# Optimization experiments

Measured on AMD Instinct MI355X. Metric: run time of the kernel, lower is better.

## Reference

```python
import jax, jax.numpy as jnp
import numpy as np


def sparsemax(z):
    """Euclidean projection onto the simplex (Martins & Astudillo 2016).
    z: (..., L) logits -> sparse probability vectors of same shape.
    """
    L = z.shape[-1]
    z_sorted = jnp.flip(jnp.sort(z, axis=-1), axis=-1)          # descending
    cum = jnp.cumsum(z_sorted, axis=-1)
    k = jnp.arange(1, L + 1, dtype=z.dtype)                     # 1..L
    support = 1.0 + k * z_sorted > cum                          # prefix-true mask
    k_max = jnp.sum(support, axis=-1, keepdims=True).astype(z.dtype)
    # sum of z_sorted over the support == cumsum at the last supported index
    cum_at_k = jnp.sum(jnp.where(support, z_sorted, 0.0), axis=-1, keepdims=True)
    tau = (cum_at_k - 1.0) / k_max
    return jnp.maximum(z - tau, 0.0)


def setup_inputs() -> dict:
    key = jax.random.key(0)
    k1, k2 = jax.random.split(key)
    B, K, L = 64, 16, 16384
    attention_logits = jax.random.normal(k1, (B, K, L), dtype=jnp.float32)
    rationale_mask = (jax.random.uniform(k2, (B, L)) < 0.1).astype(jnp.float32)
    return {"attention_logits": attention_logits, "rationale_mask": rationale_mask}


def reference(attention_logits, rationale_mask):
    # normalize the rationale mask into a probability target q
    q = rationale_mask / jnp.clip(
        jnp.sum(rationale_mask, axis=-1, keepdims=True), 1e-12, None
    )  # (B, L)
    p = sparsemax(attention_logits)            # (B, K, L), all heads batched
    diff = p - q[:, None, :]                   # broadcast target over heads
    # per-(example, head) loss 0.5*||p - q||^2, then mean over batch and heads
    # (= mean over heads of per-head batch means, as in the torch loop)
    return 0.5 * jnp.mean(jnp.sum(diff * diff, axis=-1))
```

## Files before the change

kernel.cpp:

```cpp
#include <hip/hip_runtime.h>

#define BB 64
#define KK 16
#define LL 16384
#define CAP 2048
#define NROW (BB * KK)

__device__ unsigned int g_done = 0;

__global__ __launch_bounds__(256, 4) void fused_sparsemax_loss(
    const float* __restrict__ logits, const float* __restrict__ mask,
    float* __restrict__ ws, float* __restrict__ out) {
  int row = blockIdx.x;
  int b = row >> 4;
  int kseg = row & 15;
  const float* z = logits + (size_t)row * LL;
  const float* m = mask + (size_t)b * LL;
  const float4* zv = reinterpret_cast<const float4*>(z);
  const float4* mv = reinterpret_cast<const float4*>(m);
  int t = threadIdx.x;
  int wave = t >> 6, lane = t & 63;

  __shared__ float lds_val[CAP];
  __shared__ int   lds_idx[CAP];
  __shared__ float fin[4 * NROW];
  __shared__ int   lds_n;
  __shared__ float lds_f[4], lds_s[4], lds_sq[4];
  __shared__ float red[4], red2[4];
  __shared__ int   lds_last;

  if (t == 0) lds_n = 0;

  float4 v[16];
#pragma unroll
  for (int j = 0; j < 16; ++j) v[j] = zv[j * 256 + t];
  float4 w = mv[kseg * 256 + t];

  float mx0 = -3.0e38f, mx1 = -3.0e38f, mx2 = -3.0e38f, mx3 = -3.0e38f;
#pragma unroll
  for (int j = 0; j < 4; ++j) {
    mx0 = fmaxf(mx0, fmaxf(fmaxf(v[4*j+0].x, v[4*j+0].y), fmaxf(v[4*j+0].z, v[4*j+0].w)));
    mx1 = fmaxf(mx1, fmaxf(fmaxf(v[4*j+1].x, v[4*j+1].y), fmaxf(v[4*j+1].z, v[4*j+1].w)));
    mx2 = fmaxf(mx2, fmaxf(fmaxf(v[4*j+2].x, v[4*j+2].y), fmaxf(v[4*j+2].z, v[4*j+2].w)));
    mx3 = fmaxf(mx3, fmaxf(fmaxf(v[4*j+3].x, v[4*j+3].y), fmaxf(v[4*j+3].z, v[4*j+3].w)));
  }
  float vmax = fmaxf(fmaxf(mx0, mx1), fmaxf(mx2, mx3));
  float ms  = w.x + w.y + w.z + w.w;
  float msq = w.x * w.x + w.y * w.y + w.z * w.z + w.w * w.w;
  for (int off = 32; off; off >>= 1) {
    vmax = fmaxf(vmax, __shfl_xor(vmax, off));
    ms  += __shfl_xor(ms, off);
    msq += __shfl_xor(msq, off);
  }
  if (lane == 0) { lds_f[wave] = vmax; lds_s[wave] = ms; lds_sq[wave] = msq; }
  __syncthreads();
  float zmax = fmaxf(fmaxf(lds_f[0], lds_f[1]), fmaxf(lds_f[2], lds_f[3]));
  float thr = zmax - 1.0f;
  if (t == 0) {
    ws[2 * NROW + 2 * row]     = lds_s[0] + lds_s[1] + lds_s[2] + lds_s[3];
    ws[2 * NROW + 2 * row + 1] = lds_sq[0] + lds_sq[1] + lds_sq[2] + lds_sq[3];
  }

#pragma unroll
  for (int j = 0; j < 16; ++j) {
    int base = (j * 256 + t) * 4;
    float vv[4] = {v[j].x, v[j].y, v[j].z, v[j].w};
#pragma unroll
    for (int e = 0; e < 4; ++e) {
      if (vv[e] > thr) {
        int pos = atomicAdd(&lds_n, 1);
        if (pos < CAP) { lds_val[pos] = vv[e]; lds_idx[pos] = base + e; }
      }
    }
  }
  __syncthreads();
  int n = lds_n;

  float a1 = 0.f, t2 = 0.f;

  if (n <= 64) {
    if (wave == 0) {
      float c = (lane < n) ? lds_val[lane] : -3.0e38f;
#pragma unroll
      for (int size = 2; size <= 64; size <<= 1) {
#pragma unroll
        for (int stride = size >> 1; stride > 0; stride >>= 1) {
          float other = __shfl_xor(c, stride);
          bool dirDesc = ((lane & size) == 0);
          bool takeMax = (dirDesc == ((lane & stride) == 0));
          float mn = fminf(c, other), mxv = fmaxf(c, other);
          c = takeMax ? mxv : mn;
        }
      }
      float cum = c;
#pragma unroll
      for (int off = 1; off < 64; off <<= 1) {
        float y = __shfl_up(cum, off);
        if (lane >= off) cum += y;
      }
      bool sup = (lane < n) && (1.0f + (float)(lane + 1) * c > cum);
      unsigned long long bal = __ballot(sup);
      int k = __popcll(bal);
      float S = sup ? c : 0.f;
      for (int off = 32; off; off >>= 1) S += __shfl_xor(S, off);
      float tau = (S - 1.0f) / (float)k;

      float aa1 = 0.f, aa2 = 0.f;
      if (lane < n) {
        float val = lds_val[lane];
        float p = fmaxf(val - tau, 0.f);
        if (p > 0.f) {
          aa1 = p * p;
          aa2 = p * m[lds_idx[lane]];
        }
      }
      for (int off = 32; off; off >>= 1) {
        aa1 += __shfl_xor(aa1, off);
        aa2 += __shfl_xor(aa2, off);
      }
      a1 = aa1; t2 = aa2;
    }
  } else if (n <= CAP) {
    if (wave == 0) {
      int nj = (n + 63) >> 6;
      float lo = thr, hi = zmax;
      for (int it = 0; it < 30; ++it) {
        float mid = 0.5f * (lo + hi);
        float s = 0.f;
        for (int j = 0; j < nj; ++j) {
          int i = j * 64 + lane;
          float cc = (i < n) ? lds_val[i] : -3.0e38f;
          s += fmaxf(cc - mid, 0.f);
        }
        for (int off = 32; off; off >>= 1) s += __shfl_xor(s, off);
        if (s >= 1.0f) lo = mid; else hi = mid;
      }
      float S = 0.f, kc = 0.f;
      for (int j = 0; j < nj; ++j) {
        int i = j * 64 + lane;
        float cc = (i < n) ? lds_val[i] : -3.0e38f;
        if (cc > lo) { S += cc; kc += 1.f; }
      }
      for (int off = 32; off; off >>= 1) {
        S  += __shfl_xor(S, off);
        kc += __shfl_xor(kc, off);
      }
      float tau = (S - 1.0f) / kc;

      float aa1 = 0.f, aa2 = 0.f;
      for (int j = 0; j < nj; ++j) {
        int i = j * 64 + lane;
        if (i < n) {
          float p = fmaxf(lds_val[i] - tau, 0.f);
          if (p > 0.f) {
            aa1 += p * p;
            aa2 += p * m[lds_idx[i]];
          }
        }
      }
      for (int off = 32; off; off >>= 1) {
        aa1 += __shfl_xor(aa1, off);
        aa2 += __shfl_xor(aa2, off);
      }
      a1 = aa1; t2 = aa2;
    }
  } else {
    float lo = thr, hi = zmax;
    for (int it = 0; it < 30; ++it) {
      float mid = 0.5f * (lo + hi);
      float s = 0.f;
      for (int j = 0; j < 16; ++j) {
        float4 vv = zv[j * 256 + t];
        s += fmaxf(vv.x - mid, 0.f) + fmaxf(vv.y - mid, 0.f) +
             fmaxf(vv.z - mid, 0.f) + fmaxf(vv.w - mid, 0.f);
      }
      for (int off = 32; off; off >>= 1) s += __shfl_xor(s, off);
      __syncthreads();
      if (lane == 0) red[wave] = s;
      __syncthreads();
      float tot = red[0] + red[1] + red[2] + red[3];
      if (tot >= 1.0f) lo = mid; else hi = mid;
    }
    float S = 0.f, kc = 0.f;
    for (int j = 0; j < 16; ++j) {
      float4 vv4 = zv[j * 256 + t];
      float vv[4] = {vv4.x, vv4.y, vv4.z, vv4.w};
      for (int e = 0; e < 4; ++e)
        if (vv[e] > lo) { S += vv[e]; kc += 1.f; }
    }
    for (int off = 32; off; off >>= 1) {
      S  += __shfl_xor(S, off);
      kc += __shfl_xor(kc, off);
    }
    __syncthreads();
    if (lane == 0) { red[wave] = S; red2[wave] = kc; }
    __syncthreads();
    S  = red[0] + red[1] + red[2] + red[3];
    kc = red2[0] + red2[1] + red2[2] + red2[3];
    float tau = (S - 1.0f) / kc;

    float aa1 = 0.f, aa2 = 0.f;
    for (int j = 0; j < 16; ++j) {
      int base = (j * 256 + t) * 4;
      float4 vv4 = zv[j * 256 + t];
      float vv[4] = {vv4.x, vv4.y, vv4.z, vv4.w};
      for (int e = 0; e < 4; ++e) {
        float p = fmaxf(vv[e] - tau, 0.f);
        if (p > 0.f) {
          aa1 += p * p;
          aa2 += p * m[base + e];
        }
      }
    }
    for (int off = 32; off; off >>= 1) {
      aa1 += __shfl_xor(aa1, off);
      aa2 += __shfl_xor(aa2, off);
    }
    __syncthreads();
    if (lane == 0) { red[wave] = aa1; red2[wave] = aa2; }
    __syncthreads();
    if (t == 0) {
      a1 = red[0] + red[1] + red[2] + red[3];
      t2 = red2[0] + red2[1] + red2[2] + red2[3];
    }
  }

  if (t == 0) {
    ws[2 * row]     = a1;
    ws[2 * row + 1] = t2;
    __threadfence();
    unsigned old = atomicAdd(&g_done, 1u);
    int last = (old == NROW - 1);
    lds_last = last;
    if (last) atomicExch(&g_done, 0u);
  }
  __syncthreads();

  if (lds_last) {
    __threadfence();
    const float4* wv4 = reinterpret_cast<const float4*>(ws);
    float4* fin4 = reinterpret_cast<float4*>(fin);
#pragma unroll
    for (int j = 0; j < 4; ++j) fin4[j * 256 + t] = wv4[j * 256 + t];
    __syncthreads();

    float acc = 0.f;
    if (t < 64) {
      float S = 0.f, SQ = 0.f;
#pragma unroll
      for (int kk = 0; kk < 16; ++kk) {
        S  += fin[2 * NROW + 2 * (t * 16 + kk)];
        SQ += fin[2 * NROW + 2 * (t * 16 + kk) + 1];
      }
      float inv = 1.0f / fmaxf(S, 1e-12f);
      float sumq2 = SQ * inv * inv;
      acc = 16.0f * sumq2;
#pragma unroll
      for (int kk = 0; kk < 16; ++kk) {
        float A1 = fin[2 * (t * 16 + kk)];
        float T2 = fin[2 * (t * 16 + kk) + 1];
        acc += A1 - 2.0f * inv * T2;
      }
    }
    if (wave == 0) {
      for (int off = 32; off; off >>= 1) acc += __shfl_xor(acc, off);
      if (t == 0) out[0] = acc * (0.5f / (float)(BB * KK));
    }
  }
}

extern "C" void kernel_launch(void* const* d_in, const int* in_sizes, int n_in,
                              void* d_out, int out_size, void* d_ws, size_t ws_size,
                              hipStream_t stream) {
  const float* logits = (const float*)d_in[0];
  const float* mask   = (const float*)d_in[1];
  float* ws  = (float*)d_ws;
  float* out = (float*)d_out;

  fused_sparsemax_loss<<<NROW, 256, 0, stream>>>(logits, mask, ws, out);
}
```

Measured before the change: 124.4 us.

## Split fused kernel into partial and combine kernels with 512-thread blocks

Doubles threads per row block to 512, so each thread keeps 8 float4 values in registers instead of 16. It also halves the LDS candidate capacity and drops the large shared finalization buffer, which lowers per-block LDS and register use and allows more resident blocks. The last-block atomic counter is replaced by a separate single-wave combine kernel, which adds a second launch and its dependency gap on the stream. An empty asm barrier is added to force the loads to issue early.

```diff
diff --git a/kernel.cpp b/kernel.cpp
--- a/kernel.cpp
+++ b/kernel.cpp
@@ -3,14 +3,13 @@
 #define BB 64
 #define KK 16
 #define LL 16384
-#define CAP 2048
+#define CAP 1024
 #define NROW (BB * KK)
-
-__device__ unsigned int g_done = 0;
-
-__global__ __launch_bounds__(256, 4) void fused_sparsemax_loss(
+#define TPB 512
+
+__global__ __launch_bounds__(TPB, 8) void sparsemax_partial(
     const float* __restrict__ logits, const float* __restrict__ mask,
-    float* __restrict__ ws, float* __restrict__ out) {
+    float* __restrict__ ws) {
   int row = blockIdx.x;
   int b = row >> 4;
   int kseg = row & 15;
@@ -23,28 +22,29 @@
 
   __shared__ float lds_val[CAP];
   __shared__ int   lds_idx[CAP];
-  __shared__ float fin[4 * NROW];
   __shared__ int   lds_n;
-  __shared__ float lds_f[4], lds_s[4], lds_sq[4];
-  __shared__ float red[4], red2[4];
-  __shared__ int   lds_last;
+  __shared__ float lds_f[8], lds_s[8], lds_sq[8];
+  __shared__ float red[8], red2[8];
 
   if (t == 0) lds_n = 0;
 
-  float4 v[16];
-#pragma unroll
-  for (int j = 0; j < 16; ++j) v[j] = zv[j * 256 + t];
-  float4 w = mv[kseg * 256 + t];
-
-  float mx0 = -3.0e38f, mx1 = -3.0e38f, mx2 = -3.0e38f, mx3 = -3.0e38f;
+  float4 v[8];
+#pragma unroll
+  for (int j = 0; j < 8; ++j) v[j] = zv[j * TPB + t];
+  float4 w = make_float4(0.f, 0.f, 0.f, 0.f);
+  if (t < 256) w = mv[kseg * 256 + t];
+
+#pragma unroll
+  for (int j = 0; j < 8; ++j)
+    asm volatile("" : "+v"(v[j].x), "+v"(v[j].y), "+v"(v[j].z), "+v"(v[j].w));
+
+  float mx0 = -3.0e38f, mx1 = -3.0e38f;
 #pragma unroll
   for (int j = 0; j < 4; ++j) {
-    mx0 = fmaxf(mx0, fmaxf(fmaxf(v[4*j+0].x, v[4*j+0].y), fmaxf(v[4*j+0].z, v[4*j+0].w)));
-    mx1 = fmaxf(mx1, fmaxf(fmaxf(v[4*j+1].x, v[4*j+1].y), fmaxf(v[4*j+1].z, v[4*j+1].w)));
-    mx2 = fmaxf(mx2, fmaxf(fmaxf(v[4*j+2].x, v[4*j+2].y), fmaxf(v[4*j+2].z, v[4*j+2].w)));
-    mx3 = fmaxf(mx3, fmaxf(fmaxf(v[4*j+3].x, v[4*j+3].y), fmaxf(v[4*j+3].z, v[4*j+3].w)));
-  }
-  float vmax = fmaxf(fmaxf(mx0, mx1), fmaxf(mx2, mx3));
+    mx0 = fmaxf(mx0, fmaxf(fmaxf(v[2*j+0].x, v[2*j+0].y), fmaxf(v[2*j+0].z, v[2*j+0].w)));
+    mx1 = fmaxf(mx1, fmaxf(fmaxf(v[2*j+1].x, v[2*j+1].y), fmaxf(v[2*j+1].z, v[2*j+1].w)));
+  }
+  float vmax = fmaxf(mx0, mx1);
   float ms  = w.x + w.y + w.z + w.w;
   float msq = w.x * w.x + w.y * w.y + w.z * w.z + w.w * w.w;
   for (int off = 32; off; off >>= 1) {
@@ -54,16 +54,21 @@
   }
   if (lane == 0) { lds_f[wave] = vmax; lds_s[wave] = ms; lds_sq[wave] = msq; }
   __syncthreads();
-  float zmax = fmaxf(fmaxf(lds_f[0], lds_f[1]), fmaxf(lds_f[2], lds_f[3]));
+  float zmax = lds_f[0];
+#pragma unroll
+  for (int ww = 1; ww < 8; ++ww) zmax = fmaxf(zmax, lds_f[ww]);
   float thr = zmax - 1.0f;
   if (t == 0) {
-    ws[2 * NROW + 2 * row]     = lds_s[0] + lds_s[1] + lds_s[2] + lds_s[3];
-    ws[2 * NROW + 2 * row + 1] = lds_sq[0] + lds_sq[1] + lds_sq[2] + lds_sq[3];
-  }
-
-#pragma unroll
-  for (int j = 0; j < 16; ++j) {
-    int base = (j * 256 + t) * 4;
+    float S = 0.f, SQ = 0.f;
+#pragma unroll
+    for (int ww = 0; ww < 8; ++ww) { S += lds_s[ww]; SQ += lds_sq[ww]; }
+    ws[2 * NROW + 2 * row]     = S;
+    ws[2 * NROW + 2 * row + 1] = SQ;
+  }
+
+#pragma unroll
+  for (int j = 0; j < 8; ++j) {
+    int base = (j * TPB + t) * 4;
     float vv[4] = {v[j].x, v[j].y, v[j].z, v[j].w};
 #pragma unroll
     for (int e = 0; e < 4; ++e) {
@@ -75,8 +80,6 @@
   }
   __syncthreads();
   int n = lds_n;
-
-  float a1 = 0.f, t2 = 0.f;
 
   if (n <= 64) {
     if (wave == 0) {
@@ -118,7 +121,7 @@
         aa1 += __shfl_xor(aa1, off);
         aa2 += __shfl_xor(aa2, off);
       }
-      a1 = aa1; t2 = aa2;
+      if (lane == 0) { ws[2 * row] = aa1; ws[2 * row + 1] = aa2; }
     }
   } else if (n <= CAP) {
     if (wave == 0) {
@@ -162,15 +165,15 @@
         aa1 += __shfl_xor(aa1, off);
         aa2 += __shfl_xor(aa2, off);
       }
-      a1 = aa1; t2 = aa2;
+      if (lane == 0) { ws[2 * row] = aa1; ws[2 * row + 1] = aa2; }
     }
   } else {
     float lo = thr, hi = zmax;
     for (int it = 0; it < 30; ++it) {
       float mid = 0.5f * (lo + hi);
       float s = 0.f;
-      for (int j = 0; j < 16; ++j) {
-        float4 vv = zv[j * 256 + t];
+      for (int j = 0; j < 8; ++j) {
+        float4 vv = zv[j * TPB + t];
         s += fmaxf(vv.x - mid, 0.f) + fmaxf(vv.y - mid, 0.f) +
              fmaxf(vv.z - mid, 0.f) + fmaxf(vv.w - mid, 0.f);
       }
@@ -178,12 +181,14 @@
       __syncthreads();
       if (lane == 0) red[wave] = s;
       __syncthreads();
-      float tot = red[0] + red[1] + red[2] + red[3];
+      float tot = 0.f;
+#pragma unroll
+      for (int ww = 0; ww < 8; ++ww) tot += red[ww];
       if (tot >= 1.0f) lo = mid; else hi = mid;
     }
     float S = 0.f, kc = 0.f;
-    for (int j = 0; j < 16; ++j) {
-      float4 vv4 = zv[j * 256 + t];
+    for (int j = 0; j < 8; ++j) {
+      float4 vv4 = zv[j * TPB + t];
       float vv[4] = {vv4.x, vv4.y, vv4.z, vv4.w};
       for (int e = 0; e < 4; ++e)
         if (vv[e] > lo) { S += vv[e]; kc += 1.f; }
@@ -195,14 +200,15 @@
     __syncthreads();
     if (lane == 0) { red[wave] = S; red2[wave] = kc; }
     __syncthreads();
-    S  = red[0] + red[1] + red[2] + red[3];
-    kc = red2[0] + red2[1] + red2[2] + red2[3];
+    S = 0.f; kc = 0.f;
+#pragma unroll
+    for (int ww = 0; ww < 8; ++ww) { S += red[ww]; kc += red2[ww]; }
     float tau = (S - 1.0f) / kc;
 
     float aa1 = 0.f, aa2 = 0.f;
-    for (int j = 0; j < 16; ++j) {
-      int base = (j * 256 + t) * 4;
-      float4 vv4 = zv[j * 256 + t];
+    for (int j = 0; j < 8; ++j) {
+      int base = (j * TPB + t) * 4;
+      float4 vv4 = zv[j * TPB + t];
       float vv[4] = {vv4.x, vv4.y, vv4.z, vv4.w};
       for (int e = 0; e < 4; ++e) {
         float p = fmaxf(vv[e] - tau, 0.f);
@@ -220,53 +226,34 @@
     if (lane == 0) { red[wave] = aa1; red2[wave] = aa2; }
     __syncthreads();
     if (t == 0) {
-      a1 = red[0] + red[1] + red[2] + red[3];
-      t2 = red2[0] + red2[1] + red2[2] + red2[3];
-    }
-  }
-
-  if (t == 0) {
-    ws[2 * row]     = a1;
-    ws[2 * row + 1] = t2;
-    __threadfence();
-    unsigned old = atomicAdd(&g_done, 1u);
-    int last = (old == NROW - 1);
-    lds_last = last;
-    if (last) atomicExch(&g_done, 0u);
-  }
-  __syncthreads();
-
-  if (lds_last) {
-    __threadfence();
-    const float4* wv4 = reinterpret_cast<const float4*>(ws);
-    float4* fin4 = reinterpret_cast<float4*>(fin);
-#pragma unroll
-    for (int j = 0; j < 4; ++j) fin4[j * 256 + t] = wv4[j * 256 + t];
-    __syncthreads();
-
-    float acc = 0.f;
-    if (t < 64) {
-      float S = 0.f, SQ = 0.f;
-#pragma unroll
-      for (int kk = 0; kk < 16; ++kk) {
-        S  += fin[2 * NROW + 2 * (t * 16 + kk)];
-        SQ += fin[2 * NROW + 2 * (t * 16 + kk) + 1];
-      }
-      float inv = 1.0f / fmaxf(S, 1e-12f);
-      float sumq2 = SQ * inv * inv;
-      acc = 16.0f * sumq2;
-#pragma unroll
-      for (int kk = 0; kk < 16; ++kk) {
-        float A1 = fin[2 * (t * 16 + kk)];
-        float T2 = fin[2 * (t * 16 + kk) + 1];
-        acc += A1 - 2.0f * inv * T2;
-      }
-    }
-    if (wave == 0) {
-      for (int off = 32; off; off >>= 1) acc += __shfl_xor(acc, off);
-      if (t == 0) out[0] = acc * (0.5f / (float)(BB * KK));
-    }
-  }
+      aa1 = 0.f; aa2 = 0.f;
+#pragma unroll
+      for (int ww = 0; ww < 8; ++ww) { aa1 += red[ww]; aa2 += red2[ww]; }
+      ws[2 * row] = aa1;
+      ws[2 * row + 1] = aa2;
+    }
+  }
+}
+
+__global__ __launch_bounds__(64) void combine_kernel(
+    const float* __restrict__ ws, float* __restrict__ out) {
+  int t = threadIdx.x;
+  float S = 0.f, SQ = 0.f;
+#pragma unroll
+  for (int kk = 0; kk < 16; ++kk) {
+    S  += ws[2 * NROW + 2 * (t * 16 + kk)];
+    SQ += ws[2 * NROW + 2 * (t * 16 + kk) + 1];
+  }
+  float inv = 1.0f / fmaxf(S, 1e-12f);
+  float acc = 16.0f * SQ * inv * inv;
+#pragma unroll
+  for (int kk = 0; kk < 16; ++kk) {
+    float A1 = ws[2 * (t * 16 + kk)];
+    float T2 = ws[2 * (t * 16 + kk) + 1];
+    acc += A1 - 2.0f * inv * T2;
+  }
+  for (int off = 32; off; off >>= 1) acc += __shfl_xor(acc, off);
+  if (t == 0) out[0] = acc * (0.5f / (float)(BB * KK));
 }
 
 extern "C" void kernel_launch(void* const* d_in, const int* in_sizes, int n_in,
@@ -277,5 +264,6 @@
   float* ws  = (float*)d_ws;
   float* out = (float*)d_out;
 
-  fused_sparsemax_loss<<<NROW, 256, 0, stream>>>(logits, mask, ws, out);
+  sparsemax_partial<<<NROW, TPB, 0, stream>>>(logits, mask, ws);
+  combine_kernel<<<1, 64, 0, stream>>>(ws, out);
 }
```

Measured after the change: 122.7 us. Within noise of the previous version (-1.4%).
